# Performance work log

Measured on AMD Instinct MI355X. Metric: run time of the kernel, lower is better.

Reference implementation:

```python
import jax, jax.numpy as jnp
import numpy as np
import math

B, S, D, H = 2, 2048, 1024, 16
HD = D // H  # 64


def setup_inputs() -> dict:
    key = jax.random.key(0)
    ks = jax.random.split(key, 12)
    s = 1.0 / math.sqrt(D)
    inp = {
        "x": jax.random.normal(ks[0], (B, S, D), dtype=jnp.float32),
        "Wq": jax.random.normal(ks[1], (D, D), dtype=jnp.float32) * s,
        "bq": jnp.zeros((D,), dtype=jnp.float32),
        "Wk": jax.random.normal(ks[2], (D, D), dtype=jnp.float32) * s,
        "bk": jnp.zeros((D,), dtype=jnp.float32),
        "Wv": jax.random.normal(ks[3], (D, D), dtype=jnp.float32) * s,
        "bv": jnp.zeros((D,), dtype=jnp.float32),
        "Wo": jax.random.normal(ks[4], (D, D), dtype=jnp.float32) * s,
        "bo": jnp.zeros((D,), dtype=jnp.float32),
        "cross_modal_weights": jnp.ones((3, 3), dtype=jnp.float32),
        "mask": jax.random.randint(ks[5], (B, S, S), 0, 2, dtype=jnp.int32),
        "modality_info": jax.random.randint(ks[6], (B, S), 0, 3, dtype=jnp.int64),
    }
    return inp


def reference(x, Wq, bq, Wk, bk, Wv, bv, Wo, bo, cross_modal_weights, mask, modality_info):
    b, s, d = x.shape
    # QKV projections -> [b, H, s, HD]
    q = (x @ Wq + bq).reshape(b, s, H, HD).transpose(0, 2, 1, 3)
    k = (x @ Wk + bk).reshape(b, s, H, HD).transpose(0, 2, 1, 3)
    v = (x @ Wv + bv).reshape(b, s, H, HD).transpose(0, 2, 1, 3)
    scores = jnp.einsum("bhqd,bhkd->bhqk", q, k) / math.sqrt(HD)
    # modality bias: torch uses .item() -> detached scalar
    modality_bias = jax.lax.stop_gradient(jnp.mean(cross_modal_weights))
    scores = scores + modality_bias
    # user mask [b, s, s] broadcast over heads; masked_fill(mask==0, -1e9)
    scores = jnp.where(mask[:, None, :, :] == 0, jnp.float32(-1e9), scores)
    attn = jax.nn.softmax(scores, axis=-1)
    # dropout_rate = 0.0 (eval) -> identity
    ctx = jnp.einsum("bhqk,bhkd->bhqd", attn, v)
    ctx = ctx.transpose(0, 2, 1, 3).reshape(b, s, d)
    return ctx @ Wo + bo
```

## Files before the change

### kernel.cpp

```cpp
#include <hip/hip_runtime.h>
#include <math.h>

#define Bdim 2
#define Sdim 2048
#define Ddim 1024
#define Hnum 16
#define HDdim 64
#define Kdim 1024

using short8   = __attribute__((ext_vector_type(8))) short;
using ushort8  = __attribute__((ext_vector_type(8))) unsigned short;
using ushort4v = __attribute__((ext_vector_type(4))) unsigned short;
using floatx4  = __attribute__((ext_vector_type(4))) float;
using half4    = __attribute__((ext_vector_type(4))) _Float16;

__device__ __forceinline__ unsigned short f2bf(float f) {
    __bf16 b = (__bf16)f;
    return __builtin_bit_cast(unsigned short, b);
}

__device__ __forceinline__ void async_ld16(const unsigned short* g, unsigned short* l) {
    __builtin_amdgcn_global_load_lds(
        (const __attribute__((address_space(1))) unsigned int*)(g),
        (__attribute__((address_space(3))) unsigned int*)(l), 16, 0, 0);
}

__global__ __launch_bounds__(256) void convert_x_kernel(
    const float* __restrict__ x, unsigned short* __restrict__ xb)
{
    size_t i = ((size_t)blockIdx.x * 256 + threadIdx.x) * 8;
    float4 a = *(const float4*)(x + i);
    float4 b = *(const float4*)(x + i + 4);
    ushort8 o;
    o[0] = f2bf(a.x); o[1] = f2bf(a.y); o[2] = f2bf(a.z); o[3] = f2bf(a.w);
    o[4] = f2bf(b.x); o[5] = f2bf(b.y); o[6] = f2bf(b.z); o[7] = f2bf(b.w);
    *(ushort8*)(xb + i) = o;
}

__global__ __launch_bounds__(256) void transpose_w_kernel(
    const float* __restrict__ Wq, const float* __restrict__ Wk,
    const float* __restrict__ Wv, const float* __restrict__ Wo,
    unsigned short* __restrict__ Wt)
{
    __shared__ float tile[64][65];
    const int z = blockIdx.z;
    const float* W = (z == 0) ? Wq : (z == 1) ? Wk : (z == 2) ? Wv : Wo;
    unsigned short* outp = Wt + (size_t)z * Kdim * Ddim;
    const int n0 = blockIdx.x * 64;
    const int k0 = blockIdx.y * 64;
    const int t = threadIdx.x;
#pragma unroll
    for (int i = 0; i < 4; ++i) {
        int flat = i * 256 + t;
        int r = flat >> 4;
        int c = (flat & 15) * 4;
        float4 v = *(const float4*)(W + (size_t)(k0 + r) * Ddim + n0 + c);
        tile[r][c] = v.x; tile[r][c + 1] = v.y; tile[r][c + 2] = v.z; tile[r][c + 3] = v.w;
    }
    __syncthreads();
#pragma unroll
    for (int i = 0; i < 16; ++i) {
        int flat = i * 256 + t;
        int n = flat >> 6;
        int k = flat & 63;
        outp[(size_t)(n0 + n) * Kdim + k0 + k] = f2bf(tile[k][n]);
    }
}

__global__ __launch_bounds__(256) void pack_mask_kernel(
    const int* __restrict__ mask, unsigned long long* __restrict__ packed)
{
    const int t    = threadIdx.x;
    const int lane = t & 63;
    const int l15  = lane & 15;
    const int quad = lane >> 4;
    const unsigned int widx = blockIdx.x * 4 + (t >> 6);
    const int r  = widx & 3;
    const int kb = (widx >> 2) & 127;
    const int qg = (widx >> 9) & 127;
    const int b  = widx >> 16;
    int mv = mask[((size_t)(b * Sdim) + qg * 16 + l15) * Sdim + kb * 16 + quad * 4 + r];
    unsigned long long bits = __ballot(mv != 0);
    if (lane == 0) packed[widx] = bits;
}

#define MFMA_NORM(MT, NT) acc[MT][NT] = __builtin_amdgcn_mfma_f32_16x16x32_bf16(af[MT], bfr[NT], acc[MT][NT], 0, 0, 0)
#define MFMA_SWAP(MT, NT) acc[MT][NT] = __builtin_amdgcn_mfma_f32_16x16x32_bf16(bfr[NT], af[MT], acc[MT][NT], 0, 0, 0)

#define GEMM_KLOOP(APTR, WPTR, NT_TILES, MFMA_STMT)                              \
    for (int kt = 0; kt < 16; ++kt) {                                            \
        const int k0 = kt * 64;                                                  \
        __syncthreads();                                                         \
        _Pragma("unroll")                                                        \
        for (int i = 0; i < 4; ++i) {                                            \
            int flat = i * 256 + t;                                              \
            int row  = flat >> 3;                                                \
            int cg   = (flat & 7) ^ (row & 7);                                   \
            async_ld16(APTR + (size_t)(m0 + row) * Kdim + k0 + cg * 8,           \
                       As + flat * 8);                                           \
        }                                                                        \
        _Pragma("unroll")                                                        \
        for (int i = 0; i < NT_TILES; ++i) {                                     \
            int flat = i * 256 + t;                                              \
            int row  = flat >> 3;                                                \
            int cg   = (flat & 7) ^ (row & 7);                                   \
            async_ld16(WPTR + (size_t)row * Kdim + k0 + cg * 8,                  \
                       Bs + flat * 8);                                           \
        }                                                                        \
        __syncthreads();                                                         \
        _Pragma("unroll")                                                        \
        for (int ks = 0; ks < 2; ++ks) {                                         \
            short8 af[4], bfr[NT_TILES];                                         \
            _Pragma("unroll")                                                    \
            for (int mt = 0; mt < 4; ++mt) {                                     \
                int row = wm * 64 + mt * 16 + l15;                               \
                int ch  = (ks * 4 + quad) ^ (row & 7);                           \
                af[mt] = *(const short8*)(As + row * 64 + ch * 8);               \
            }                                                                    \
            _Pragma("unroll")                                                    \
            for (int nt = 0; nt < NT_TILES; ++nt) {                              \
                int row = wn * (NT_TILES * 16) + nt * 16 + l15;                  \
                int ch  = (ks * 4 + quad) ^ (row & 7);                           \
                bfr[nt] = *(const short8*)(Bs + row * 64 + ch * 8);              \
            }                                                                    \
            _Pragma("unroll")                                                    \
            for (int mt = 0; mt < 4; ++mt)                                       \
                _Pragma("unroll")                                                \
                for (int nt = 0; nt < NT_TILES; ++nt)                            \
                    MFMA_STMT(mt, nt);                                           \
        }                                                                        \
    }

__global__ __launch_bounds__(256) void qkv_mfma_kernel(
    const unsigned short* __restrict__ A, const unsigned short* __restrict__ Wt,
    const float* __restrict__ bq, const float* __restrict__ bk, const float* __restrict__ bv,
    unsigned short* __restrict__ qo, unsigned short* __restrict__ ko, _Float16* __restrict__ vto)
{
    __shared__ __align__(16) unsigned short As[128 * 64];
    __shared__ __align__(16) unsigned short Bs[128 * 64];
    const int n0   = blockIdx.x * 128;
    const int m0   = blockIdx.y * 128;
    const int wsel = n0 >> 10;
    const int c0   = n0 & 1023;
    const unsigned short* Wp = Wt + (size_t)wsel * Kdim * Ddim + (size_t)c0 * Kdim;

    const int t    = threadIdx.x;
    const int lane = t & 63;
    const int w    = t >> 6;
    const int quad = lane >> 4;
    const int l15  = lane & 15;
    const int wm   = w & 1;
    const int wn   = w >> 1;
    floatx4 acc[4][4];
#pragma unroll
    for (int mt = 0; mt < 4; ++mt)
#pragma unroll
        for (int nt = 0; nt < 4; ++nt) acc[mt][nt] = (floatx4){0.f, 0.f, 0.f, 0.f};

    if (wsel < 2) {
        GEMM_KLOOP(A, Wp, 4, MFMA_SWAP)
        const float* bias = wsel ? bk : bq;
        unsigned short* outp = wsel ? ko : qo;
        const float qsc = wsel ? 1.0f : 0.18033688011112042f;
#pragma unroll
        for (int mt = 0; mt < 4; ++mt) {
            int m    = m0 + wm * 64 + mt * 16 + l15;
            int bidx = m >> 11;
            int s    = m & 2047;
#pragma unroll
            for (int nt = 0; nt < 4; ++nt) {
                int c = c0 + wn * 64 + nt * 16 + quad * 4;
                float4 bb = *(const float4*)(bias + c);
                int h  = c >> 6;
                int hd = c & 63;
                ushort4v o;
                o[0] = f2bf((acc[mt][nt][0] + bb.x) * qsc);
                o[1] = f2bf((acc[mt][nt][1] + bb.y) * qsc);
                o[2] = f2bf((acc[mt][nt][2] + bb.z) * qsc);
                o[3] = f2bf((acc[mt][nt][3] + bb.w) * qsc);
                *(ushort4v*)(outp + ((size_t)(bidx * Hnum + h) * Sdim + s) * HDdim + hd) = o;
            }
        }
    } else {
        GEMM_KLOOP(A, Wp, 4, MFMA_NORM)
#pragma unroll
        for (int nt = 0; nt < 4; ++nt) {
            int c = c0 + wn * 64 + nt * 16 + l15;
            float bb = bv[c];
            int h  = c >> 6;
            int hd = c & 63;
#pragma unroll
            for (int mt = 0; mt < 4; ++mt) {
                int m    = m0 + wm * 64 + mt * 16 + quad * 4;
                int bidx = m >> 11;
                int s    = m & 2047;
                half4 o;
#pragma unroll
                for (int r = 0; r < 4; ++r) o[r] = (_Float16)(acc[mt][nt][r] + bb);
                *(half4*)(vto + ((size_t)(bidx * Hnum + h) * HDdim + hd) * Sdim + s) = o;
            }
        }
    }
}

__global__ __launch_bounds__(256) void out_mfma_kernel(
    const unsigned short* __restrict__ A, const unsigned short* __restrict__ Wt,
    const float* __restrict__ bias, float* __restrict__ out)
{
    __shared__ __align__(16) unsigned short As[128 * 64];
    __shared__ __align__(16) unsigned short Bs[64 * 64];
    const int n0 = blockIdx.x * 64;
    const int m0 = blockIdx.y * 128;
    const unsigned short* Wp = Wt + (size_t)3 * Kdim * Ddim + (size_t)n0 * Kdim;

    const int t    = threadIdx.x;
    const int lane = t & 63;
    const int w    = t >> 6;
    const int quad = lane >> 4;
    const int l15  = lane & 15;
    const int wm   = w & 1;
    const int wn   = w >> 1;
    floatx4 acc[4][2];
#pragma unroll
    for (int mt = 0; mt < 4; ++mt)
#pragma unroll
        for (int nt = 0; nt < 2; ++nt) acc[mt][nt] = (floatx4){0.f, 0.f, 0.f, 0.f};

    GEMM_KLOOP(A, Wp, 2, MFMA_SWAP)

#pragma unroll
    for (int mt = 0; mt < 4; ++mt) {
        int m = m0 + wm * 64 + mt * 16 + l15;
#pragma unroll
        for (int nt = 0; nt < 2; ++nt) {
            int c = n0 + wn * 32 + nt * 16 + quad * 4;
            float4 bb = *(const float4*)(bias + c);
            float4 o = make_float4(acc[mt][nt][0] + bb.x, acc[mt][nt][1] + bb.y,
                                   acc[mt][nt][2] + bb.z, acc[mt][nt][3] + bb.w);
            *(float4*)(out + (size_t)m * Ddim + c) = o;
        }
    }
}

__global__ __launch_bounds__(128, 2) void attn_mfma_kernel(
    const unsigned short* __restrict__ q, const unsigned short* __restrict__ k,
    const _Float16* __restrict__ vt, const unsigned long long* __restrict__ pmask,
    unsigned short* __restrict__ ctx)
{
    __shared__ __align__(16) unsigned short Ks[2][64 * 64];
    __shared__ __align__(16) _Float16       Vs[2][64 * 64];

    const int t    = threadIdx.x;
    const int w    = t >> 6;
    const int lane = t & 63;
    const int quad = lane >> 4;
    const int l15  = lane & 15;
    const int bid  = blockIdx.x;
    const int bh   = bid & 31;
    const int qseg = bid >> 5;
    const int b    = bh >> 4;
    const int h    = bh & 15;
    const int qrow0 = qseg * 64 + w * 32;

    const unsigned short* qp = q  + (size_t)bh * Sdim * HDdim;
    const unsigned short* kp = k  + (size_t)bh * Sdim * HDdim;
    const _Float16*       vp = vt + (size_t)bh * HDdim * Sdim;

    const int qg0 = __builtin_amdgcn_readfirstlane(qrow0 >> 4);
    const unsigned long long* __restrict__ pm =
        pmask + ((size_t)(b * 128 + qg0) * 128) * 4;

    short8 qf[2][2];
#pragma unroll
    for (int g = 0; g < 2; ++g)
#pragma unroll
        for (int ks = 0; ks < 2; ++ks)
            qf[g][ks] = *(const short8*)(qp + (size_t)(qrow0 + g * 16 + l15) * HDdim + ks * 32 + quad * 8);

    floatx4 acc[2][4];
    floatx4 accl[2];
#pragma unroll
    for (int g = 0; g < 2; ++g) {
        accl[g] = (floatx4){0.f, 0.f, 0.f, 0.f};
#pragma unroll
        for (int hs = 0; hs < 4; ++hs) acc[g][hs] = (floatx4){0.f, 0.f, 0.f, 0.f};
    }
    const half4 ones = {(_Float16)1.f, (_Float16)1.f, (_Float16)1.f, (_Float16)1.f};

    auto stage = [&](int buf, int key0) {
#pragma unroll
        for (int i = 0; i < 4; ++i) {
            int flat = i * 128 + t;
            int row  = flat >> 3;
            int cg   = (flat & 7) ^ (row & 7);
            async_ld16(kp + (size_t)(key0 + row) * HDdim + cg * 8, &Ks[buf][flat * 8]);
        }
#pragma unroll
        for (int i = 0; i < 4; ++i) {
            int flat = i * 128 + t;
            int row  = flat >> 3;
            int cg   = (flat & 7) ^ (row & 7);
            async_ld16((const unsigned short*)(vp + (size_t)row * Sdim + key0 + cg * 8),
                       (unsigned short*)&Vs[buf][flat * 8]);
        }
    };

    stage(0, 0);

#pragma unroll 2
    for (int kt = 0; kt < 32; ++kt) {
        const int cur = kt & 1;
        __syncthreads();
        if (kt < 31) stage(cur ^ 1, (kt + 1) * 64);

        short8 kf[2][4];
#pragma unroll
        for (int ks = 0; ks < 2; ++ks)
#pragma unroll
            for (int sub = 0; sub < 4; ++sub) {
                int row = sub * 16 + l15;
                int ch  = (ks * 4 + quad) ^ (row & 7);
                kf[ks][sub] = *(const short8*)&Ks[cur][row * 64 + ch * 8];
            }
        half4 vf[4][4];
#pragma unroll
        for (int hs = 0; hs < 4; ++hs)
#pragma unroll
            for (int c = 0; c < 4; ++c) {
                int row = hs * 16 + l15;
                int cc  = c * 2 + (quad >> 1);
                int ch  = cc ^ (row & 7);
                vf[hs][c] = *(const half4*)&Vs[cur][row * 64 + ch * 8 + (quad & 1) * 4];
            }

        floatx4 sc[2][4];
#pragma unroll
        for (int g = 0; g < 2; ++g)
#pragma unroll
            for (int sub = 0; sub < 4; ++sub) sc[g][sub] = (floatx4){0.f, 0.f, 0.f, 0.f};
#pragma unroll
        for (int ks = 0; ks < 2; ++ks)
#pragma unroll
            for (int sub = 0; sub < 4; ++sub)
#pragma unroll
                for (int g = 0; g < 2; ++g)
                    sc[g][sub] = __builtin_amdgcn_mfma_f32_16x16x32_bf16(
                        kf[ks][sub], qf[g][ks], sc[g][sub], 0, 0, 0);

        half4 pf[2][4];
#pragma unroll
        for (int g = 0; g < 2; ++g) {
            const unsigned long long* __restrict__ pg = pm + g * 512 + kt * 16;
#pragma unroll
            for (int c = 0; c < 4; ++c) {
#pragma unroll
                for (int r = 0; r < 4; ++r) {
                    float p = exp2f(sc[g][c][r]);
                    unsigned long long wmask = pg[c * 4 + r];
                    float pmv;
                    asm("v_cndmask_b32 %0, 0, %1, %2" : "=v"(pmv) : "v"(p), "s"(wmask));
                    pf[g][c][r] = (_Float16)pmv;
                }
            }
        }

#pragma unroll
        for (int c = 0; c < 4; ++c) {
#pragma unroll
            for (int hs = 0; hs < 4; ++hs)
#pragma unroll
                for (int g = 0; g < 2; ++g)
                    acc[g][hs] = __builtin_amdgcn_mfma_f32_16x16x16f16(
                        vf[hs][c], pf[g][c], acc[g][hs], 0, 0, 0);
#pragma unroll
            for (int g = 0; g < 2; ++g)
                accl[g] = __builtin_amdgcn_mfma_f32_16x16x16f16(
                    ones, pf[g][c], accl[g], 0, 0, 0);
        }
    }

#pragma unroll
    for (int g = 0; g < 2; ++g) {
        float inv = 1.0f / fmaxf(accl[g][0], 1e-30f);
        int row = qrow0 + g * 16 + l15;
#pragma unroll
        for (int hs = 0; hs < 4; ++hs) {
            ushort4v o;
#pragma unroll
            for (int r = 0; r < 4; ++r) o[r] = f2bf(acc[g][hs][r] * inv);
            *(ushort4v*)(ctx + (size_t)(b * Sdim + row) * Ddim + h * 64 + hs * 16 + quad * 4) = o;
        }
    }
}

extern "C" void kernel_launch(void* const* d_in, const int* in_sizes, int n_in,
                              void* d_out, int out_size, void* d_ws, size_t ws_size,
                              hipStream_t stream) {
    const float* x   = (const float*)d_in[0];
    const float* Wq  = (const float*)d_in[1];
    const float* bq  = (const float*)d_in[2];
    const float* Wk  = (const float*)d_in[3];
    const float* bk  = (const float*)d_in[4];
    const float* Wv  = (const float*)d_in[5];
    const float* bv  = (const float*)d_in[6];
    const float* Wo  = (const float*)d_in[7];
    const float* bo  = (const float*)d_in[8];
    const int*  mask = (const int*)d_in[10];
    float* out = (float*)d_out;

    char* ws = (char*)d_ws;
    unsigned short* xb  = (unsigned short*)(ws);
    unsigned short* Wt  = (unsigned short*)(ws + (size_t)8  * 1048576);
    unsigned short* qb  = (unsigned short*)(ws + (size_t)16 * 1048576);
    unsigned short* kb  = (unsigned short*)(ws + (size_t)24 * 1048576);
    _Float16*       vtb = (_Float16*)     (ws + (size_t)32 * 1048576);
    unsigned long long* pmk = (unsigned long long*)(ws + (size_t)40 * 1048576);
    unsigned short* ctxb = xb;

    convert_x_kernel<<<dim3(2048), 256, 0, stream>>>(x, xb);
    transpose_w_kernel<<<dim3(16, 16, 4), 256, 0, stream>>>(Wq, Wk, Wv, Wo, Wt);
    pack_mask_kernel<<<dim3(32768), 256, 0, stream>>>(mask, pmk);
    qkv_mfma_kernel<<<dim3(24, 32), 256, 0, stream>>>(xb, Wt, bq, bk, bv, qb, kb, vtb);
    attn_mfma_kernel<<<dim3(1024), 128, 0, stream>>>(qb, kb, vtb, pmk, ctxb);
    out_mfma_kernel<<<dim3(16, 32), 256, 0, stream>>>(ctxb, Wt, bo, out);
}
```

Measured before the change: 275.5 us.

## Fuse prep kernels, vectorize mask packing, enlarge attention blocks, pack fp16 converts

Merges the x conversion, weight transpose and mask packing into one prep launch. Mask packing now does one int4 load and four ballots per wave instead of one scalar load per wave. Attention blocks grow to 256 threads covering 128 query rows, so each staged K/V tile is shared by four waves. Probability conversion uses packed cvt_pkrtz, which rounds toward zero. The aim is fewer launches, less mask-read traffic and less redundant K/V loading, at the cost of different occupancy and a slightly different fp16 rounding mode.

Result: faster. 254.6 us (-7.6%).

```diff
diff --git a/kernel.cpp b/kernel.cpp
--- a/kernel.cpp
+++ b/kernel.cpp
@@ -13,6 +13,7 @@
 using ushort4v = __attribute__((ext_vector_type(4))) unsigned short;
 using floatx4  = __attribute__((ext_vector_type(4))) float;
 using half4    = __attribute__((ext_vector_type(4))) _Float16;
+using half2v   = __attribute__((ext_vector_type(2))) _Float16;
 
 __device__ __forceinline__ unsigned short f2bf(float f) {
     __bf16 b = (__bf16)f;
@@ -25,63 +26,67 @@
         (__attribute__((address_space(3))) unsigned int*)(l), 16, 0, 0);
 }
 
-__global__ __launch_bounds__(256) void convert_x_kernel(
-    const float* __restrict__ x, unsigned short* __restrict__ xb)
-{
-    size_t i = ((size_t)blockIdx.x * 256 + threadIdx.x) * 8;
-    float4 a = *(const float4*)(x + i);
-    float4 b = *(const float4*)(x + i + 4);
-    ushort8 o;
-    o[0] = f2bf(a.x); o[1] = f2bf(a.y); o[2] = f2bf(a.z); o[3] = f2bf(a.w);
-    o[4] = f2bf(b.x); o[5] = f2bf(b.y); o[6] = f2bf(b.z); o[7] = f2bf(b.w);
-    *(ushort8*)(xb + i) = o;
-}
-
-__global__ __launch_bounds__(256) void transpose_w_kernel(
+__global__ __launch_bounds__(256) void prep_kernel(
+    const float* __restrict__ x,
     const float* __restrict__ Wq, const float* __restrict__ Wk,
     const float* __restrict__ Wv, const float* __restrict__ Wo,
-    unsigned short* __restrict__ Wt)
+    const int* __restrict__ mask,
+    unsigned short* __restrict__ xb, unsigned short* __restrict__ Wt,
+    unsigned long long* __restrict__ packed)
 {
     __shared__ float tile[64][65];
-    const int z = blockIdx.z;
-    const float* W = (z == 0) ? Wq : (z == 1) ? Wk : (z == 2) ? Wv : Wo;
-    unsigned short* outp = Wt + (size_t)z * Kdim * Ddim;
-    const int n0 = blockIdx.x * 64;
-    const int k0 = blockIdx.y * 64;
-    const int t = threadIdx.x;
-#pragma unroll
-    for (int i = 0; i < 4; ++i) {
-        int flat = i * 256 + t;
-        int r = flat >> 4;
-        int c = (flat & 15) * 4;
-        float4 v = *(const float4*)(W + (size_t)(k0 + r) * Ddim + n0 + c);
-        tile[r][c] = v.x; tile[r][c + 1] = v.y; tile[r][c + 2] = v.z; tile[r][c + 3] = v.w;
-    }
-    __syncthreads();
-#pragma unroll
-    for (int i = 0; i < 16; ++i) {
-        int flat = i * 256 + t;
-        int n = flat >> 6;
-        int k = flat & 63;
-        outp[(size_t)(n0 + n) * Kdim + k0 + k] = f2bf(tile[k][n]);
-    }
-}
-
-__global__ __launch_bounds__(256) void pack_mask_kernel(
-    const int* __restrict__ mask, unsigned long long* __restrict__ packed)
-{
-    const int t    = threadIdx.x;
-    const int lane = t & 63;
-    const int l15  = lane & 15;
-    const int quad = lane >> 4;
-    const unsigned int widx = blockIdx.x * 4 + (t >> 6);
-    const int r  = widx & 3;
-    const int kb = (widx >> 2) & 127;
-    const int qg = (widx >> 9) & 127;
-    const int b  = widx >> 16;
-    int mv = mask[((size_t)(b * Sdim) + qg * 16 + l15) * Sdim + kb * 16 + quad * 4 + r];
-    unsigned long long bits = __ballot(mv != 0);
-    if (lane == 0) packed[widx] = bits;
+    const int bid = blockIdx.x;
+    const int t   = threadIdx.x;
+
+    if (bid < 2048) {
+        size_t i = ((size_t)bid * 256 + t) * 8;
+        float4 a = *(const float4*)(x + i);
+        float4 b = *(const float4*)(x + i + 4);
+        ushort8 o;
+        o[0] = f2bf(a.x); o[1] = f2bf(a.y); o[2] = f2bf(a.z); o[3] = f2bf(a.w);
+        o[4] = f2bf(b.x); o[5] = f2bf(b.y); o[6] = f2bf(b.z); o[7] = f2bf(b.w);
+        *(ushort8*)(xb + i) = o;
+    } else if (bid < 3072) {
+        const int idx = bid - 2048;
+        const int n0 = (idx & 15) * 64;
+        const int k0 = ((idx >> 4) & 15) * 64;
+        const int z  = idx >> 8;
+        const float* W = (z == 0) ? Wq : (z == 1) ? Wk : (z == 2) ? Wv : Wo;
+        unsigned short* outp = Wt + (size_t)z * Kdim * Ddim;
+#pragma unroll
+        for (int i = 0; i < 4; ++i) {
+            int flat = i * 256 + t;
+            int r = flat >> 4;
+            int c = (flat & 15) * 4;
+            float4 v = *(const float4*)(W + (size_t)(k0 + r) * Ddim + n0 + c);
+            tile[r][c] = v.x; tile[r][c+1] = v.y; tile[r][c+2] = v.z; tile[r][c+3] = v.w;
+        }
+        __syncthreads();
+#pragma unroll
+        for (int i = 0; i < 16; ++i) {
+            int flat = i * 256 + t;
+            int n = flat >> 6;
+            int k = flat & 63;
+            outp[(size_t)(n0 + n) * Kdim + k0 + k] = f2bf(tile[k][n]);
+        }
+    } else {
+        const int lane = t & 63;
+        const int l15  = lane & 15;
+        const int quad = lane >> 4;
+        const unsigned int gid = (bid - 3072) * 4 + (t >> 6);
+        const int b  = gid >> 14;
+        const int qg = (gid >> 7) & 127;
+        const int kb = gid & 127;
+        int4 mv = *(const int4*)(mask + ((size_t)(b * Sdim) + qg * 16 + l15) * Sdim + kb * 16 + quad * 4);
+        unsigned long long w0 = __ballot(mv.x != 0);
+        unsigned long long w1 = __ballot(mv.y != 0);
+        unsigned long long w2 = __ballot(mv.z != 0);
+        unsigned long long w3 = __ballot(mv.w != 0);
+        if (lane == 0) {
+            unsigned long long* dst = packed + (size_t)gid * 4;
+            dst[0] = w0; dst[1] = w1; dst[2] = w2; dst[3] = w3;
+        }
+    }
 }
 
 #define MFMA_NORM(MT, NT) acc[MT][NT] = __builtin_amdgcn_mfma_f32_16x16x32_bf16(af[MT], bfr[NT], acc[MT][NT], 0, 0, 0)
@@ -242,7 +247,7 @@
     }
 }
 
-__global__ __launch_bounds__(128, 2) void attn_mfma_kernel(
+__global__ __launch_bounds__(256, 2) void attn_mfma_kernel(
     const unsigned short* __restrict__ q, const unsigned short* __restrict__ k,
     const _Float16* __restrict__ vt, const unsigned long long* __restrict__ pmask,
     unsigned short* __restrict__ ctx)
@@ -260,7 +265,7 @@
     const int qseg = bid >> 5;
     const int b    = bh >> 4;
     const int h    = bh & 15;
-    const int qrow0 = qseg * 64 + w * 32;
+    const int qrow0 = qseg * 128 + w * 32;
 
     const unsigned short* qp = q  + (size_t)bh * Sdim * HDdim;
     const unsigned short* kp = k  + (size_t)bh * Sdim * HDdim;
@@ -289,15 +294,15 @@
 
     auto stage = [&](int buf, int key0) {
 #pragma unroll
-        for (int i = 0; i < 4; ++i) {
-            int flat = i * 128 + t;
+        for (int i = 0; i < 2; ++i) {
+            int flat = i * 256 + t;
             int row  = flat >> 3;
             int cg   = (flat & 7) ^ (row & 7);
             async_ld16(kp + (size_t)(key0 + row) * HDdim + cg * 8, &Ks[buf][flat * 8]);
         }
 #pragma unroll
-        for (int i = 0; i < 4; ++i) {
-            int flat = i * 128 + t;
+        for (int i = 0; i < 2; ++i) {
+            int flat = i * 256 + t;
             int row  = flat >> 3;
             int cg   = (flat & 7) ^ (row & 7);
             async_ld16((const unsigned short*)(vp + (size_t)row * Sdim + key0 + cg * 8),
@@ -353,14 +358,17 @@
             const unsigned long long* __restrict__ pg = pm + g * 512 + kt * 16;
 #pragma unroll
             for (int c = 0; c < 4; ++c) {
+                float pv[4];
 #pragma unroll
                 for (int r = 0; r < 4; ++r) {
                     float p = exp2f(sc[g][c][r]);
                     unsigned long long wmask = pg[c * 4 + r];
-                    float pmv;
-                    asm("v_cndmask_b32 %0, 0, %1, %2" : "=v"(pmv) : "v"(p), "s"(wmask));
-                    pf[g][c][r] = (_Float16)pmv;
+                    asm("v_cndmask_b32 %0, 0, %1, %2" : "=v"(pv[r]) : "v"(p), "s"(wmask));
                 }
+                half2v lo = __builtin_bit_cast(half2v, __builtin_amdgcn_cvt_pkrtz(pv[0], pv[1]));
+                half2v hi = __builtin_bit_cast(half2v, __builtin_amdgcn_cvt_pkrtz(pv[2], pv[3]));
+                pf[g][c][0] = lo[0]; pf[g][c][1] = lo[1];
+                pf[g][c][2] = hi[0]; pf[g][c][3] = hi[1];
             }
         }
 
@@ -417,10 +425,8 @@
     unsigned long long* pmk = (unsigned long long*)(ws + (size_t)40 * 1048576);
     unsigned short* ctxb = xb;
 
-    convert_x_kernel<<<dim3(2048), 256, 0, stream>>>(x, xb);
-    transpose_w_kernel<<<dim3(16, 16, 4), 256, 0, stream>>>(Wq, Wk, Wv, Wo, Wt);
-    pack_mask_kernel<<<dim3(32768), 256, 0, stream>>>(mask, pmk);
+    prep_kernel<<<dim3(11264), 256, 0, stream>>>(x, Wq, Wk, Wv, Wo, mask, xb, Wt, pmk);
     qkv_mfma_kernel<<<dim3(24, 32), 256, 0, stream>>>(xb, Wt, bq, bk, bv, qb, kb, vtb);
-    attn_mfma_kernel<<<dim3(1024), 128, 0, stream>>>(qb, kb, vtb, pmk, ctxb);
+    attn_mfma_kernel<<<dim3(512), 256, 0, stream>>>(qb, kb, vtb, pmk, ctxb);
     out_mfma_kernel<<<dim3(16, 32), 256, 0, stream>>>(ctxb, Wt, bo, out);
 }
```
